# Optimization experiments

Hardware: AMD Instinct MI355X
Metric: run time of the kernel (lower is better)

Reference implementation:

```python
import jax, jax.numpy as jnp
import numpy as np

N_NODES = 100000
N_EDGES = 1600000
BN_EPS = 1e-5


def gcn_conv(x, src, dst, W, b, n_nodes):
    # DGL GraphConv, norm='both': h = D_out^{-1/2} A D_in^{-1/2} x W + b
    ones = jnp.ones(src.shape[0], dtype=x.dtype)
    deg_out = jax.ops.segment_sum(ones, src, num_segments=n_nodes)
    deg_in = jax.ops.segment_sum(ones, dst, num_segments=n_nodes)
    norm_src = jax.lax.rsqrt(jnp.maximum(deg_out, 1.0))  # [N]
    norm_dst = jax.lax.rsqrt(jnp.maximum(deg_in, 1.0))   # [N]
    # apply weight before aggregation (DGL does this when in_feats >= out_feats; math identical)
    h = (x * norm_src[:, None]) @ W                      # [N, out]
    agg = jax.ops.segment_sum(h[src], dst, num_segments=n_nodes)  # scatter-add over edges
    return agg * norm_dst[:, None] + b


def batchnorm(x, gamma, beta):
    # BatchNorm1d, training-mode math (batch statistics over node axis)
    mu = jnp.mean(x, axis=0)
    var = jnp.mean(jnp.square(x - mu), axis=0)
    return (x - mu) * jax.lax.rsqrt(var + BN_EPS) * gamma + beta


def setup_inputs() -> dict:
    key = jax.random.key(0)
    ks = jax.random.split(key, 8)
    d_in, d_h, d_out = 128, 128, 64
    return {
        "features": jax.random.normal(ks[0], (N_NODES, d_in), dtype=jnp.float32),
        "src": jax.random.randint(ks[1], (N_EDGES,), 0, N_NODES, dtype=jnp.int32),
        "dst": jax.random.randint(ks[2], (N_EDGES,), 0, N_NODES, dtype=jnp.int32),
        "W1": jax.random.normal(ks[3], (d_in, d_h), dtype=jnp.float32) / np.sqrt(d_in),
        "b1": jnp.zeros((d_h,), dtype=jnp.float32),
        "gamma1": jnp.ones((d_h,), dtype=jnp.float32),
        "beta1": jnp.zeros((d_h,), dtype=jnp.float32),
        "W2": jax.random.normal(ks[4], (d_h, d_h), dtype=jnp.float32) / np.sqrt(d_h),
        "b2": jnp.zeros((d_h,), dtype=jnp.float32),
        "W3": jax.random.normal(ks[5], (d_h, d_out), dtype=jnp.float32) / np.sqrt(d_h),
        "b3": jnp.zeros((d_out,), dtype=jnp.float32),
    }


def reference(features, src, dst, W1, b1, gamma1, beta1, W2, b2, W3, b3):
    n = features.shape[0]
    x = jax.nn.relu(gcn_conv(features, src, dst, W1, b1, n))
    x = batchnorm(x, gamma1, beta1)  # dropout = identity (eval mode)
    x = jax.nn.relu(gcn_conv(x, src, dst, W2, b2, n))
    x = gcn_conv(x, src, dst, W3, b3, n)
    return x
```

## Files before the change

kernel.cpp:

```cpp
#include <hip/hip_runtime.h>

#define NFEAT 128

constexpr int HCHUNK = 32768;
constexpr int HBLOCKS = 128;

__global__ __launch_bounds__(256) void hist_k(const int* __restrict__ idx, int ne, int n,
                                              unsigned int* __restrict__ partials) {
    __shared__ unsigned int cnt[HCHUNK / 2];
    int b = blockIdx.x;
    int p = blockIdx.y;
    int per = (ne + HBLOCKS - 1) / HBLOCKS;
    int e0 = b * per, e1 = min(e0 + per, ne);
    int base = p * HCHUNK;
    for (int i = threadIdx.x; i < HCHUNK / 2; i += 256) cnt[i] = 0;
    __syncthreads();
    for (int e = e0 + threadIdx.x; e < e1; e += 256) {
        int d = idx[e] - base;
        if ((unsigned)d < (unsigned)HCHUNK) {
            atomicAdd(&cnt[d >> 1], 1u << ((d & 1) * 16));
        }
    }
    __syncthreads();
    unsigned int* dstp = partials + ((size_t)p * HBLOCKS + b) * (HCHUNK / 2);
    for (int i = threadIdx.x; i < HCHUNK / 2; i += 256) dstp[i] = cnt[i];
}

template <bool PFX>
__global__ void sum_prefix_k(unsigned int* __restrict__ partials, int* __restrict__ deg,
                             int n, int npass) {
    int slot = blockIdx.x * 256 + threadIdx.x;
    int total = npass * (HCHUNK / 2);
    if (slot >= total) return;
    int p = slot / (HCHUNK / 2);
    int j2 = slot - p * (HCHUNK / 2);
    unsigned int* base = partials + (size_t)p * HBLOCKS * (HCHUNK / 2) + j2;
    unsigned lo = 0, hi = 0;
    for (int b = 0; b < HBLOCKS; b++) {
        unsigned v = base[(size_t)b * (HCHUNK / 2)];
        if (PFX) base[(size_t)b * (HCHUNK / 2)] = lo | (hi << 16);
        lo += v & 0xffffu;
        hi += v >> 16;
    }
    int node = p * HCHUNK + 2 * j2;
    if (node < n) deg[node] = (int)lo;
    if (node + 1 < n) deg[node + 1] = (int)hi;
}

__global__ void norms_k(const int* __restrict__ dout, const int* __restrict__ din,
                        float* __restrict__ ns, float* __restrict__ nd, int n) {
    int i = blockIdx.x * 256 + threadIdx.x;
    if (i < n) {
        ns[i] = rsqrtf(fmaxf((float)dout[i], 1.f));
        nd[i] = rsqrtf(fmaxf((float)din[i], 1.f));
    }
}

__global__ void scan1_k(const int* __restrict__ deg, int* __restrict__ rp,
                        int* __restrict__ partials, int n) {
    __shared__ int tmp[256];
    int t = threadIdx.x;
    int i = blockIdx.x * 256 + t;
    int v = (i < n) ? deg[i] : 0;
    tmp[t] = v;
    __syncthreads();
    int val = v;
    for (int off = 1; off < 256; off <<= 1) {
        int add = (t >= off) ? tmp[t - off] : 0;
        __syncthreads();
        val += add;
        tmp[t] = val;
        __syncthreads();
    }
    if (i < n) rp[i] = val - v;
    if (t == 255) partials[blockIdx.x] = val;
}

__global__ void scan2_k(int* __restrict__ partials, int nb) {
    __shared__ int tmp[512];
    int t = threadIdx.x;
    int v = (t < nb) ? partials[t] : 0;
    tmp[t] = v;
    __syncthreads();
    int val = v;
    for (int off = 1; off < 512; off <<= 1) {
        int add = (t >= off) ? tmp[t - off] : 0;
        __syncthreads();
        val += add;
        tmp[t] = val;
        __syncthreads();
    }
    if (t < nb) partials[t] = val - v;
}

__global__ void scan3_k(int* __restrict__ rp, const int* __restrict__ partials,
                        const int* __restrict__ deg, int n) {
    int i = blockIdx.x * 256 + threadIdx.x;
    if (i < n) {
        int r = rp[i] + partials[blockIdx.x];
        rp[i] = r;
        if (i == n - 1) rp[n] = r + deg[i];
    }
}

__global__ __launch_bounds__(256) void fill2_k(const int* __restrict__ src,
                                               const int* __restrict__ dst,
                                               const int* __restrict__ rp,
                                               const unsigned int* __restrict__ prefix,
                                               int* __restrict__ esrc, int ne, int n) {
    __shared__ unsigned int cnt[HCHUNK / 2];
    int b = blockIdx.x;
    int p = blockIdx.y;
    int per = (ne + HBLOCKS - 1) / HBLOCKS;
    int e0 = b * per, e1 = min(e0 + per, ne);
    int base = p * HCHUNK;
    for (int i = threadIdx.x; i < HCHUNK / 2; i += 256) cnt[i] = 0;
    __syncthreads();
    const unsigned int* pf = prefix + ((size_t)p * HBLOCKS + b) * (HCHUNK / 2);
    for (int e = e0 + threadIdx.x; e < e1; e += 256) {
        int d = dst[e] - base;
        if ((unsigned)d < (unsigned)HCHUNK) {
            int sh = (d & 1) * 16;
            unsigned old = atomicAdd(&cnt[d >> 1], 1u << sh);
            int rank = (int)((old >> sh) & 0xffffu);
            int pos = rp[base + d] + (int)((pf[d >> 1] >> sh) & 0xffffu) + rank;
            esrc[pos] = src[e];
        }
    }
}

template <int NCOL, bool HAS_V>
__global__ __launch_bounds__(256) void gemm_k(
    const float* __restrict__ X, const float* __restrict__ W,
    const float* __restrict__ rs, const float* __restrict__ vvec,
    float* __restrict__ H, int n) {
    constexpr int BK = 32;
    constexpr int CG = NCOL / 4;
    constexpr int RG = 256 / CG;
    constexpr int BM = RG * 4;
    __shared__ float Xs[BK][BM + 4];
    __shared__ float Ws[BK][NCOL];
    int tid = threadIdx.x;
    int tx = tid % CG;
    int ty = tid / CG;
    int row0 = blockIdx.x * BM;
    float acc[4][4] = {};
    for (int k0 = 0; k0 < NFEAT; k0 += BK) {
        for (int idx = tid; idx < BK * NCOL; idx += 256) {
            int k = idx / NCOL, c = idx % NCOL;
            Ws[k][c] = W[(k0 + k) * NCOL + c];
        }
        for (int idx = tid; idx < BM * BK; idx += 256) {
            int m = idx / BK, k = idx % BK;
            int gm = row0 + m;
            Xs[k][m] = (gm < n) ? X[(size_t)gm * NFEAT + k0 + k] * rs[gm] : 0.f;
        }
        __syncthreads();
#pragma unroll
        for (int k = 0; k < BK; k++) {
            float4 a = *(const float4*)&Xs[k][ty * 4];
            float4 b = *(const float4*)&Ws[k][tx * 4];
            float av[4] = {a.x, a.y, a.z, a.w};
            float bv[4] = {b.x, b.y, b.z, b.w};
#pragma unroll
            for (int i = 0; i < 4; i++)
#pragma unroll
                for (int j = 0; j < 4; j++) acc[i][j] += av[i] * bv[j];
        }
        __syncthreads();
    }
#pragma unroll
    for (int i = 0; i < 4; i++) {
        int gm = row0 + ty * 4 + i;
        if (gm < n) {
            float4 o;
            o.x = acc[i][0]; o.y = acc[i][1]; o.z = acc[i][2]; o.w = acc[i][3];
            if (HAS_V) {
                float sc = rs[gm];
                o.x += sc * vvec[tx * 4 + 0];
                o.y += sc * vvec[tx * 4 + 1];
                o.z += sc * vvec[tx * 4 + 2];
                o.w += sc * vvec[tx * 4 + 3];
            }
            *(float4*)&H[(size_t)gm * NCOL + tx * 4] = o;
        }
    }
}

template <int F, bool RELU>
__global__ void agg_k(const float* __restrict__ H, const int* __restrict__ rp,
                      const int* __restrict__ esrc, const float* __restrict__ nd,
                      const float* __restrict__ bias, float* __restrict__ out) {
    int node = blockIdx.x;
    int c = threadIdx.x;
    int e0 = rp[node], e1 = rp[node + 1];
    float acc = 0.f;
    int e = e0;
    for (; e + 4 <= e1; e += 4) {
        int s0 = esrc[e], s1 = esrc[e + 1], s2 = esrc[e + 2], s3 = esrc[e + 3];
        float v0 = H[(size_t)s0 * F + c];
        float v1 = H[(size_t)s1 * F + c];
        float v2 = H[(size_t)s2 * F + c];
        float v3 = H[(size_t)s3 * F + c];
        acc += (v0 + v1) + (v2 + v3);
    }
    for (; e < e1; e++) acc += H[(size_t)esrc[e] * F + c];
    float val = acc * nd[node] + bias[c];
    if (RELU) val = fmaxf(val, 0.f);
    out[(size_t)node * F + c] = val;
}

constexpr int CSB = 1024;

__global__ __launch_bounds__(256) void colstats1_k(const float* __restrict__ X,
                                                   float* __restrict__ psum,
                                                   float* __restrict__ psq, int n) {
    __shared__ float sh[256];
    int t = threadIdx.x;
    int c = t & 127;
    int half = t >> 7;
    int rows_per = (n + CSB - 1) / CSB;
    int r0 = blockIdx.x * rows_per;
    int r1 = min(r0 + rows_per, n);
    float s = 0.f, sq = 0.f;
    for (int r = r0 + half; r < r1; r += 2) {
        float v = X[(size_t)r * 128 + c];
        s += v;
        sq += v * v;
    }
    sh[t] = s;
    __syncthreads();
    if (half == 0) psum[(size_t)c * CSB + blockIdx.x] = s + sh[t + 128];
    __syncthreads();
    sh[t] = sq;
    __syncthreads();
    if (half == 0) psq[(size_t)c * CSB + blockIdx.x] = sq + sh[t + 128];
}

__global__ __launch_bounds__(256) void colstats2_k(const float* __restrict__ psum,
                                                   const float* __restrict__ psq,
                                                   float* __restrict__ colsum,
                                                   float* __restrict__ colsq) {
    __shared__ float sh[256];
    int c = blockIdx.x;
    int t = threadIdx.x;
    float s = 0.f, sq = 0.f;
#pragma unroll
    for (int i = 0; i < CSB / 256; i++) {
        s += psum[(size_t)c * CSB + i * 256 + t];
        sq += psq[(size_t)c * CSB + i * 256 + t];
    }
    sh[t] = s;
    __syncthreads();
    for (int off = 128; off > 0; off >>= 1) {
        if (t < off) sh[t] += sh[t + off];
        __syncthreads();
    }
    if (t == 0) colsum[c] = sh[0];
    __syncthreads();
    sh[t] = sq;
    __syncthreads();
    for (int off = 128; off > 0; off >>= 1) {
        if (t < off) sh[t] += sh[t + off];
        __syncthreads();
    }
    if (t == 0) colsq[c] = sh[0];
}

__global__ void bn_prep_k(const float* __restrict__ colsum, const float* __restrict__ colsq,
                          const float* __restrict__ gamma, const float* __restrict__ beta,
                          const float* __restrict__ W2, float* __restrict__ W2p,
                          float* __restrict__ v2, float n) {
    __shared__ float s_s[128], s_t[128];
    int c = threadIdx.x;
    float mu = colsum[c] / n;
    float var = colsq[c] / n - mu * mu;
    float s = gamma[c] * rsqrtf(var + 1e-5f);
    float t = beta[c] - mu * s;
    s_s[c] = s;
    s_t[c] = t;
    __syncthreads();
    float acc = 0.f;
    for (int k = 0; k < 128; k++) {
        float w = W2[k * 128 + c];
        W2p[k * 128 + c] = s_s[k] * w;
        acc += s_t[k] * w;
    }
    v2[c] = acc;
}

extern "C" void kernel_launch(void* const* d_in, const int* in_sizes, int n_in,
                              void* d_out, int out_size, void* d_ws, size_t ws_size,
                              hipStream_t stream) {
    const float* feat = (const float*)d_in[0];
    const int* src = (const int*)d_in[1];
    const int* dst = (const int*)d_in[2];
    const float* W1 = (const float*)d_in[3];
    const float* b1 = (const float*)d_in[4];
    const float* gamma1 = (const float*)d_in[5];
    const float* beta1 = (const float*)d_in[6];
    const float* W2 = (const float*)d_in[7];
    const float* b2 = (const float*)d_in[8];
    const float* W3 = (const float*)d_in[9];
    const float* b3 = (const float*)d_in[10];
    float* out = (float*)d_out;

    int n = in_sizes[0] / NFEAT;
    int ne = in_sizes[1];
    int npass = (n + HCHUNK - 1) / HCHUNK;

    char* ws = (char*)d_ws;
    size_t off = 0;
    auto carve = [&](size_t bytes) -> void* {
        void* p = ws + off;
        off += (bytes + 255) & ~(size_t)255;
        return p;
    };
    float* h    = (float*)carve((size_t)n * NFEAT * 4);
    float* x    = (float*)carve((size_t)n * NFEAT * 4);
    int* esrc   = (int*)carve((size_t)ne * 4);
    int* dout_  = (int*)carve((size_t)n * 4);
    int* din_   = (int*)carve((size_t)n * 4);
    float* ns   = (float*)carve((size_t)n * 4);
    float* ndv  = (float*)carve((size_t)n * 4);
    int* rp     = (int*)carve((size_t)(n + 1) * 4);
    int* parts  = (int*)carve(512 * 4);
    float* psum = (float*)carve((size_t)128 * CSB * 4);
    float* psq  = (float*)carve((size_t)128 * CSB * 4);
    float* colsum = (float*)carve(128 * 4);
    float* colsq  = (float*)carve(128 * 4);
    float* W2p  = (float*)carve(128 * 128 * 4);
    float* v2   = (float*)carve(128 * 4);

    unsigned int* hpart = (unsigned int*)h;

    int nbl = (n + 255) / 256;
    int sbl = (npass * (HCHUNK / 2) + 255) / 256;
    dim3 hgrid(HBLOCKS, npass);

    hist_k<<<hgrid, 256, 0, stream>>>(src, ne, n, hpart);
    sum_prefix_k<false><<<sbl, 256, 0, stream>>>(hpart, dout_, n, npass);
    hist_k<<<hgrid, 256, 0, stream>>>(dst, ne, n, hpart);
    sum_prefix_k<true><<<sbl, 256, 0, stream>>>(hpart, din_, n, npass);

    norms_k<<<nbl, 256, 0, stream>>>(dout_, din_, ns, ndv, n);
    scan1_k<<<nbl, 256, 0, stream>>>(din_, rp, parts, n);
    scan2_k<<<1, 512, 0, stream>>>(parts, nbl);
    scan3_k<<<nbl, 256, 0, stream>>>(rp, parts, din_, n);
    fill2_k<<<hgrid, 256, 0, stream>>>(src, dst, rp, hpart, esrc, ne, n);

    gemm_k<128, false><<<(n + 31) / 32, 256, 0, stream>>>(feat, W1, ns, nullptr, h, n);
    agg_k<128, true><<<n, 128, 0, stream>>>(h, rp, esrc, ndv, b1, x);

    colstats1_k<<<CSB, 256, 0, stream>>>(x, psum, psq, n);
    colstats2_k<<<128, 256, 0, stream>>>(psum, psq, colsum, colsq);
    bn_prep_k<<<1, 128, 0, stream>>>(colsum, colsq, gamma1, beta1, W2, W2p, v2, (float)n);

    gemm_k<128, true><<<(n + 31) / 32, 256, 0, stream>>>(x, W2p, ns, v2, h, n);
    agg_k<128, true><<<n, 128, 0, stream>>>(h, rp, esrc, ndv, b2, x);

    gemm_k<64, false><<<(n + 63) / 64, 256, 0, stream>>>(x, W3, ns, nullptr, h, n);
    agg_k<64, false><<<n, 64, 0, stream>>>(h, rp, esrc, ndv, b3, out);
}
```

Before: 598.3 us.

## Shard aggregation by feature column slices across XCD-interleaved blocks

Replaces the one-block-per-node aggregation with 256-thread blocks that each handle 8 nodes using 32-lane column shards. Block IDs are mapped so that the low 3 bits (the XCD round-robin on MI355X) choose a feature shard, so each XCD gathers only a fixed 32-column slice of H. The intent is to shrink each XCD's L2 working set for the random gathers and to cut block-launch overhead. In exchange, each gather reads only 128 bytes per row, and the edge indices and row pointers are reread once per shard.

```diff
diff --git a/kernel.cpp b/kernel.cpp
--- a/kernel.cpp
+++ b/kernel.cpp
@@ -188,11 +188,24 @@
 }
 
 template <int F, bool RELU>
-__global__ void agg_k(const float* __restrict__ H, const int* __restrict__ rp,
-                      const int* __restrict__ esrc, const float* __restrict__ nd,
-                      const float* __restrict__ bias, float* __restrict__ out) {
-    int node = blockIdx.x;
-    int c = threadIdx.x;
+__global__ __launch_bounds__(256) void agg2_k(const float* __restrict__ H,
+                                              const int* __restrict__ rp,
+                                              const int* __restrict__ esrc,
+                                              const float* __restrict__ nd,
+                                              const float* __restrict__ bias,
+                                              float* __restrict__ out, int n) {
+    constexpr int NSH = F / 32;
+    constexpr int XPS = 8 / NSH;
+    constexpr int NPB = 8;
+    int bid = blockIdx.x;
+    int x = bid & 7;
+    int g = bid >> 3;
+    int shard = x / XPS;
+    int sub = x % XPS;
+    int node = (g * XPS + sub) * NPB + (threadIdx.x >> 5);
+    if (node >= n) return;
+    int lane = threadIdx.x & 31;
+    int c = shard * 32 + lane;
     int e0 = rp[node], e1 = rp[node + 1];
     float acc = 0.f;
     int e = e0;
@@ -349,16 +362,20 @@
     scan3_k<<<nbl, 256, 0, stream>>>(rp, parts, din_, n);
     fill2_k<<<hgrid, 256, 0, stream>>>(src, dst, rp, hpart, esrc, ne, n);
 
+    int nodeblocks = (n + 7) / 8;
+    int grid128 = 8 * ((nodeblocks + 1) / 2);
+    int grid64  = 8 * ((nodeblocks + 3) / 4);
+
     gemm_k<128, false><<<(n + 31) / 32, 256, 0, stream>>>(feat, W1, ns, nullptr, h, n);
-    agg_k<128, true><<<n, 128, 0, stream>>>(h, rp, esrc, ndv, b1, x);
+    agg2_k<128, true><<<grid128, 256, 0, stream>>>(h, rp, esrc, ndv, b1, x, n);
 
     colstats1_k<<<CSB, 256, 0, stream>>>(x, psum, psq, n);
     colstats2_k<<<128, 256, 0, stream>>>(psum, psq, colsum, colsq);
     bn_prep_k<<<1, 128, 0, stream>>>(colsum, colsq, gamma1, beta1, W2, W2p, v2, (float)n);
 
     gemm_k<128, true><<<(n + 31) / 32, 256, 0, stream>>>(x, W2p, ns, v2, h, n);
-    agg_k<128, true><<<n, 128, 0, stream>>>(h, rp, esrc, ndv, b2, x);
+    agg2_k<128, true><<<grid128, 256, 0, stream>>>(h, rp, esrc, ndv, b2, x, n);
 
     gemm_k<64, false><<<(n + 63) / 64, 256, 0, stream>>>(x, W3, ns, nullptr, h, n);
-    agg_k<64, false><<<n, 64, 0, stream>>>(h, rp, esrc, ndv, b3, out);
-}
+    agg2_k<64, false><<<grid64, 256, 0, stream>>>(h, rp, esrc, ndv, b3, out, n);
+}
```

After: 679.8 us. 1.14x slower.

## Aggregate one node per wavefront with float2 loads and 8-way unroll

Applied to the files above, without the earlier changes.

Replaces the per-node aggregation kernel, which used one block of 128 or 64 threads per node, with a kernel that packs four nodes per 256-thread block, one 64-lane wavefront per node. For 128 features each lane loads a float2, and the edge loop is unrolled by 8 so more independent gathers are in flight. This cuts block-launch overhead and the half-filled wavefronts of the F=64 case, and raises memory-level parallelism on the random row gathers. In exchange each lane keeps more loads in flight, which raises register pressure.

```diff
diff --git a/kernel.cpp b/kernel.cpp
--- a/kernel.cpp
+++ b/kernel.cpp
@@ -188,26 +188,59 @@
 }
 
 template <int F, bool RELU>
-__global__ void agg_k(const float* __restrict__ H, const int* __restrict__ rp,
-                      const int* __restrict__ esrc, const float* __restrict__ nd,
-                      const float* __restrict__ bias, float* __restrict__ out) {
-    int node = blockIdx.x;
-    int c = threadIdx.x;
+__global__ __launch_bounds__(256) void agg3_k(const float* __restrict__ H,
+                                              const int* __restrict__ rp,
+                                              const int* __restrict__ esrc,
+                                              const float* __restrict__ nd,
+                                              const float* __restrict__ bias,
+                                              float* __restrict__ out, int n) {
+    constexpr int VW = F / 64;
+    int node = blockIdx.x * 4 + (threadIdx.x >> 6);
+    if (node >= n) return;
+    int lane = threadIdx.x & 63;
     int e0 = rp[node], e1 = rp[node + 1];
-    float acc = 0.f;
+    float ax = 0.f, ay = 0.f;
     int e = e0;
-    for (; e + 4 <= e1; e += 4) {
-        int s0 = esrc[e], s1 = esrc[e + 1], s2 = esrc[e + 2], s3 = esrc[e + 3];
-        float v0 = H[(size_t)s0 * F + c];
-        float v1 = H[(size_t)s1 * F + c];
-        float v2 = H[(size_t)s2 * F + c];
-        float v3 = H[(size_t)s3 * F + c];
-        acc += (v0 + v1) + (v2 + v3);
-    }
-    for (; e < e1; e++) acc += H[(size_t)esrc[e] * F + c];
-    float val = acc * nd[node] + bias[c];
-    if (RELU) val = fmaxf(val, 0.f);
-    out[(size_t)node * F + c] = val;
+    for (; e + 8 <= e1; e += 8) {
+        int s[8];
+#pragma unroll
+        for (int j = 0; j < 8; j++) s[j] = esrc[e + j];
+#pragma unroll
+        for (int j = 0; j < 8; j++) {
+            if (VW == 2) {
+                float2 v = *(const float2*)(H + (size_t)s[j] * F + lane * 2);
+                ax += v.x;
+                ay += v.y;
+            } else {
+                ax += H[(size_t)s[j] * F + lane];
+            }
+        }
+    }
+    for (; e < e1; e++) {
+        int s = esrc[e];
+        if (VW == 2) {
+            float2 v = *(const float2*)(H + (size_t)s * F + lane * 2);
+            ax += v.x;
+            ay += v.y;
+        } else {
+            ax += H[(size_t)s * F + lane];
+        }
+    }
+    float sc = nd[node];
+    if (VW == 2) {
+        float2 o;
+        o.x = ax * sc + bias[lane * 2];
+        o.y = ay * sc + bias[lane * 2 + 1];
+        if (RELU) {
+            o.x = fmaxf(o.x, 0.f);
+            o.y = fmaxf(o.y, 0.f);
+        }
+        *(float2*)(out + (size_t)node * F + lane * 2) = o;
+    } else {
+        float o = ax * sc + bias[lane];
+        if (RELU) o = fmaxf(o, 0.f);
+        out[(size_t)node * F + lane] = o;
+    }
 }
 
 constexpr int CSB = 1024;
@@ -349,16 +382,18 @@
     scan3_k<<<nbl, 256, 0, stream>>>(rp, parts, din_, n);
     fill2_k<<<hgrid, 256, 0, stream>>>(src, dst, rp, hpart, esrc, ne, n);
 
+    int agrid = (n + 3) / 4;
+
     gemm_k<128, false><<<(n + 31) / 32, 256, 0, stream>>>(feat, W1, ns, nullptr, h, n);
-    agg_k<128, true><<<n, 128, 0, stream>>>(h, rp, esrc, ndv, b1, x);
+    agg3_k<128, true><<<agrid, 256, 0, stream>>>(h, rp, esrc, ndv, b1, x, n);
 
     colstats1_k<<<CSB, 256, 0, stream>>>(x, psum, psq, n);
     colstats2_k<<<128, 256, 0, stream>>>(psum, psq, colsum, colsq);
     bn_prep_k<<<1, 128, 0, stream>>>(colsum, colsq, gamma1, beta1, W2, W2p, v2, (float)n);
 
     gemm_k<128, true><<<(n + 31) / 32, 256, 0, stream>>>(x, W2p, ns, v2, h, n);
-    agg_k<128, true><<<n, 128, 0, stream>>>(h, rp, esrc, ndv, b2, x);
+    agg3_k<128, true><<<agrid, 256, 0, stream>>>(h, rp, esrc, ndv, b2, x, n);
 
     gemm_k<64, false><<<(n + 63) / 64, 256, 0, stream>>>(x, W3, ns, nullptr, h, n);
-    agg_k<64, false><<<n, 64, 0, stream>>>(h, rp, esrc, ndv, b3, out);
-}
+    agg3_k<64, false><<<agrid, 256, 0, stream>>>(h, rp, esrc, ndv, b3, out, n);
+}
```

New measurement: 614.8 us. 2.7% more time.
